# Performance work log

Measured on AMD Instinct MI355X. Metric: run time of the kernel, lower is better.

## Reference

```python
import jax, jax.numpy as jnp
import numpy as np

B, T_IN, T_OUT = 64, 512, 500
N_MEL, ENC_DIM, ATT_DIM = 80, 512, 128
ATT_RNN, DEC_RNN, PRENET = 1024, 1024, 256
N_FILT, KSIZE = 32, 31
PAD = (KSIZE - 1) // 2


def setup_inputs() -> dict:
    key = jax.random.key(0)
    ks = jax.random.split(key, 20)
    g = lambda i, shape, s: jax.random.normal(ks[i], shape, jnp.float32) * s
    return {
        'memory': g(0, (B, T_IN, ENC_DIM), 1.0),
        'decoder_inputs': g(1, (B, N_MEL, T_OUT), 1.0),
        'memory_lengths': jax.random.randint(ks[2], (B,), T_IN // 2, T_IN + 1).astype(jnp.int32),
        'prenet_w1': g(3, (PRENET, N_MEL), 0.05),
        'prenet_w2': g(4, (PRENET, PRENET), 0.05),
        'att_wih': g(5, (4 * ATT_RNN, PRENET + ENC_DIM), 0.02),
        'att_whh': g(6, (4 * ATT_RNN, ATT_RNN), 0.02),
        'att_bih': jnp.zeros((4 * ATT_RNN,), jnp.float32),
        'att_bhh': jnp.zeros((4 * ATT_RNN,), jnp.float32),
        'wq': g(7, (ATT_DIM, ATT_RNN), 0.03),
        'wm': g(8, (ATT_DIM, ENC_DIM), 0.03),
        'v': g(9, (ATT_DIM,), 0.05),
        'loc_conv': g(10, (N_FILT, 2, KSIZE), 0.05),
        'loc_dense': g(11, (ATT_DIM, N_FILT), 0.05),
        'dec_wih': g(12, (4 * DEC_RNN, ATT_RNN + ENC_DIM), 0.02),
        'dec_whh': g(13, (4 * DEC_RNN, DEC_RNN), 0.02),
        'dec_bih': jnp.zeros((4 * DEC_RNN,), jnp.float32),
        'dec_bhh': jnp.zeros((4 * DEC_RNN,), jnp.float32),
        'proj_w': g(14, (N_MEL, DEC_RNN + ENC_DIM), 0.02),
        'proj_b': jnp.zeros((N_MEL,), jnp.float32),
        'gate_w': g(15, (1, DEC_RNN + ENC_DIM), 0.02),
        'gate_b': jnp.zeros((1,), jnp.float32),
    }


def _lstm_cell(x, h, c, wih, whh, bih, bhh):
    gates = x @ wih.T + bih + h @ whh.T + bhh
    i, f, g, o = jnp.split(gates, 4, axis=-1)
    c_new = jax.nn.sigmoid(f) * c + jax.nn.sigmoid(i) * jnp.tanh(g)
    h_new = jax.nn.sigmoid(o) * jnp.tanh(c_new)
    return h_new, c_new


def _forward(memory, decoder_inputs, memory_lengths, prenet_w1, prenet_w2,
             att_wih, att_whh, att_bih, att_bhh, wq, wm, v, loc_conv, loc_dense,
             dec_wih, dec_whh, dec_bih, dec_bhh, proj_w, proj_b, gate_w, gate_b):
    # padding mask: True at padded encoder positions
    mask = jnp.arange(T_IN)[None, :] >= memory_lengths[:, None]  # [B, T_in]
    processed_memory = memory @ wm.T  # [B, T_in, ATT_DIM]

    # parse decoder inputs -> [T_out, B, N_MEL]; prepend all-zero go frame
    di = jnp.transpose(decoder_inputs, (2, 0, 1))
    di = jnp.concatenate([jnp.zeros((1, B, N_MEL), di.dtype), di], axis=0)

    # prenet (dropout p=0.5 is always active in the original; deterministic key)
    dk1, dk2 = jax.random.split(jax.random.key(42))
    x = jax.nn.relu(di @ prenet_w1.T)
    x = x * jax.random.bernoulli(dk1, 0.5, x.shape).astype(x.dtype) * 2.0
    x = jax.nn.relu(x @ prenet_w2.T)
    x = x * jax.random.bernoulli(dk2, 0.5, x.shape).astype(x.dtype) * 2.0  # [T_out+1, B, PRENET]

    def step(carry, x_t):
        ah, ac, dh, dc, aw, awc, ctx = carry
        # attention LSTM
        ah, ac = _lstm_cell(jnp.concatenate([x_t, ctx], -1), ah, ac,
                            att_wih, att_whh, att_bih, att_bhh)
        # location-sensitive attention
        awcat = jnp.stack([aw, awc], axis=1)  # [B, 2, T_in]
        loc = jax.lax.conv_general_dilated(awcat, loc_conv, (1,), [(PAD, PAD)],
                                           dimension_numbers=('NCH', 'OIH', 'NCH'))  # [B, F, T_in]
        loc = jnp.einsum('bft,af->bta', loc, loc_dense)  # [B, T_in, ATT_DIM]
        pq = (ah @ wq.T)[:, None, :]  # [B, 1, ATT_DIM]
        energies = jnp.tanh(pq + loc + processed_memory) @ v  # [B, T_in]
        energies = jnp.where(mask, -jnp.inf, energies)
        aw = jax.nn.softmax(energies, axis=1)
        ctx = jnp.einsum('bt,btd->bd', aw, memory)
        awc = awc + aw
        # decoder LSTM
        dh, dc = _lstm_cell(jnp.concatenate([ah, ctx], -1), dh, dc,
                            dec_wih, dec_whh, dec_bih, dec_bhh)
        dhc = jnp.concatenate([dh, ctx], -1)  # [B, DEC_RNN+ENC_DIM]
        mel = dhc @ proj_w.T + proj_b  # [B, N_MEL]
        gate = (dhc @ gate_w.T + gate_b)[:, 0]  # [B]
        return (ah, ac, dh, dc, aw, awc, ctx), (mel, gate, aw)

    z = lambda *s: jnp.zeros(s, jnp.float32)
    init = (z(B, ATT_RNN), z(B, ATT_RNN), z(B, DEC_RNN), z(B, DEC_RNN),
            z(B, T_IN), z(B, T_IN), z(B, ENC_DIM))
    _, (mels, gates, aws) = jax.lax.scan(step, init, x[:T_OUT])
    mel_outputs = jnp.transpose(mels, (1, 0, 2)).reshape(B, -1, N_MEL)  # [B, T_out, N_MEL]
    gate_outputs = gates.T  # [B, T_out]
    alignments = jnp.transpose(aws, (1, 0, 2))  # [B, T_out, T_in]
    return mel_outputs, gate_outputs, alignments


def reference(memory, decoder_inputs, memory_lengths, prenet_w1, prenet_w2,
              att_wih, att_whh, att_bih, att_bhh, wq, wm, v, loc_conv, loc_dense,
              dec_wih, dec_whh, dec_bih, dec_bhh, proj_w, proj_b, gate_w, gate_b):
    return _forward(memory, decoder_inputs, memory_lengths, prenet_w1, prenet_w2,
                    att_wih, att_whh, att_bih, att_bhh, wq, wm, v, loc_conv, loc_dense,
                    dec_wih, dec_whh, dec_bih, dec_bhh, proj_w, proj_b, gate_w, gate_b)
```

## Files before the change

kernel.cpp:

```cpp
#include <hip/hip_runtime.h>
#include <cstdint>
#include <cstddef>

#define NB    64
#define TIN   512
#define TOUT  500
#define NMEL  80
#define ENC   512
#define ATTD  128
#define ARNN  1024
#define DRNN  1024
#define PREN  256
#define NFILT 32
#define KSZ   31
#define CPAD  15

#define MEL_OFF  0
#define GATE_OFF 2560000
#define ALGN_OFF 2592000

#define X_SZ      8192000
#define PM_SZ     4194304
#define G1_SZ     1048576
#define G2_SZ     1048576
#define XATT_SZ   98304
#define XDEC_SZ   163840
#define AC_SZ     65536
#define DC_SZ     65536
#define AW_SZ     32768
#define AWC_SZ    32768
#define TAILH_SZ  49152
#define TAILL_SZ  49152
#define XDH_SZ    81920
#define XDL_SZ    81920
#define PQ_SZ     8192
#define EN_SZ     32768
#define MASK_N    8208384

#define K1TOT   1792
#define K2TOT   2560
#define NCH1    56
#define NCH2    80
#define PK1_N   14680064
#define PK2_N   20971520

typedef unsigned short u16;
typedef __attribute__((ext_vector_type(8))) short bf16x8;
typedef __attribute__((ext_vector_type(4))) float f32x4;

__device__ __forceinline__ uint32_t rotl32(uint32_t v, int r) { return (v << r) | (v >> (32 - r)); }

__device__ __forceinline__ float sigf(float x) { return 1.f / (1.f + __expf(-x)); }
__device__ __forceinline__ float tanhf_fast(float x) {
    float ax = fabsf(x);
    float t = 1.f - 2.f / (__expf(2.f * ax) + 1.f);
    return copysignf(t, x);
}

__device__ __forceinline__ void split1(float v, u16& h, u16& l) {
    uint32_t u = __float_as_uint(v);
    h = (u16)(u >> 16);
    float r = v - __uint_as_float(u & 0xFFFF0000u);
    uint32_t ru = __float_as_uint(r);
    ru += 0x7FFFu + ((ru >> 16) & 1u);
    l = (u16)(ru >> 16);
}

__device__ __forceinline__ void split8(float4 f0, float4 f1, bf16x8& h, bf16x8& l) {
    float v[8] = { f0.x, f0.y, f0.z, f0.w, f1.x, f1.y, f1.z, f1.w };
#pragma unroll
    for (int i = 0; i < 8; ++i) {
        uint32_t u = __float_as_uint(v[i]);
        h[i] = (short)(u >> 16);
        float r = v[i] - __uint_as_float(u & 0xFFFF0000u);
        uint32_t ru = __float_as_uint(r);
        ru += 0x7FFFu + ((ru >> 16) & 1u);
        l[i] = (short)(ru >> 16);
    }
}

#define MFMA16(a, b, c) __builtin_amdgcn_mfma_f32_16x16x32_bf16(a, b, c, 0, 0, 0)

__device__ void tf_block(uint32_t k1, uint32_t k2, uint32_t& x0, uint32_t& x1) {
    uint32_t ks0 = k1, ks1 = k2, ks2 = k1 ^ k2 ^ 0x1BD11BDAu;
    x0 += ks0; x1 += ks1;
#define TFR(r) { x0 += x1; x1 = rotl32(x1, r); x1 ^= x0; }
    TFR(13) TFR(15) TFR(26) TFR(6)   x0 += ks1; x1 += ks2 + 1u;
    TFR(17) TFR(29) TFR(16) TFR(24)  x0 += ks2; x1 += ks0 + 2u;
    TFR(13) TFR(15) TFR(26) TFR(6)   x0 += ks0; x1 += ks1 + 3u;
    TFR(17) TFR(29) TFR(16) TFR(24)  x0 += ks1; x1 += ks2 + 4u;
    TFR(13) TFR(15) TFR(26) TFR(6)   x0 += ks2; x1 += ks0 + 5u;
#undef TFR
}

__global__ __launch_bounds__(256) void mask_kernel(unsigned char* m1, unsigned char* m2) {
    int i = blockIdx.x * 256 + threadIdx.x;
    if (i >= MASK_N) return;
    uint32_t a0 = 0u, a1 = 0u; tf_block(0u, 42u, a0, a1);
    uint32_t b0 = 0u, b1 = 1u; tf_block(0u, 42u, b0, b1);
    uint32_t x0, x1;
    x0 = 0u; x1 = (uint32_t)i; tf_block(a0, a1, x0, x1);
    m1[i] = ((x0 ^ x1) >> 31) == 0u;
    x0 = 0u; x1 = (uint32_t)i; tf_block(b0, b1, x0, x1);
    m2[i] = ((x0 ^ x1) >> 31) == 0u;
}

__global__ __launch_bounds__(256) void prenet1_kernel(
    const float* __restrict__ dec_in, const float* __restrict__ w1,
    const unsigned char* __restrict__ m1, float* __restrict__ x)
{
    int r = blockIdx.x;
    int t = r >> 6, b = r & 63;
    int tid = threadIdx.x;
    __shared__ float ds[NMEL];
    if (tid < NMEL) ds[tid] = (t == 0) ? 0.f : dec_in[(size_t)b * 40000 + tid * 500 + (t - 1)];
    __syncthreads();
    float acc = 0.f;
    const float* w = w1 + tid * NMEL;
#pragma unroll
    for (int k = 0; k < NMEL; ++k) acc += ds[k] * w[k];
    acc = fmaxf(acc, 0.f);
    int flat = r * 256 + tid;
    x[flat] = m1[flat] ? acc * 2.f : 0.f;
}

__global__ __launch_bounds__(256) void prenet2_kernel(
    const float* __restrict__ w2, const unsigned char* __restrict__ m2, float* x)
{
    int r = blockIdx.x;
    int tid = threadIdx.x;
    __shared__ float xs[PREN];
    xs[tid] = x[r * 256 + tid];
    __syncthreads();
    float acc = 0.f;
    const float* w = w2 + tid * PREN;
#pragma unroll 8
    for (int k = 0; k < PREN; ++k) acc += xs[k] * w[k];
    acc = fmaxf(acc, 0.f);
    int flat = r * 256 + tid;
    x[flat] = m2[flat] ? acc * 2.f : 0.f;
}

__global__ __launch_bounds__(128) void pm_kernel(
    const float* __restrict__ memory, const float* __restrict__ wm, float* __restrict__ pm)
{
    int b = blockIdx.x, t = blockIdx.y;
    int tid = threadIdx.x;
    __shared__ float ms[ENC];
    for (int i = tid; i < ENC; i += 128) ms[i] = memory[(size_t)b * (TIN * ENC) + (size_t)t * ENC + i];
    __syncthreads();
    float acc = 0.f;
    const float* w = wm + tid * ENC;
#pragma unroll 8
    for (int k = 0; k < ENC; ++k) acc += ms[k] * w[k];
    pm[(size_t)b * (TIN * ATTD) + t * ATTD + tid] = acc;
}

__global__ __launch_bounds__(256) void wpack_kernel(
    const float* __restrict__ w1, int K1, const float* __restrict__ w2, int K2,
    u16* __restrict__ dst)
{
    const int K = K1 + K2;
    int idx = blockIdx.x * 256 + threadIdx.x;
    if (idx >= 4096 * K) return;
    int n = idx / K, k = idx % K;
    float v = (k < K1) ? w1[n * K1 + k] : w2[n * K2 + (k - K1)];
    u16 h, l;
    split1(v, h, l);
    int tile = n >> 4, kc = k >> 5;
    int lane = (n & 15) + (((k & 31) >> 3) << 4);
    size_t off = ((size_t)(tile * (K >> 5) + kc) * 2) * 512 + lane * 8 + (k & 7);
    dst[off] = h;
    dst[off + 512] = l;
}

struct SmemGemm { float Xs[32][68]; float Ws[32][68]; };

__device__ void gemm_phase(
    const float* __restrict__ X1, int ldx1, int kx1,
    const float* __restrict__ X2, int ldx2,
    const float* __restrict__ W1, int ldw1, int kw1,
    const float* __restrict__ W2, int ldw2,
    float* __restrict__ outp, int Kq, int blk, SmemGemm& s)
{
    const int tid = threadIdx.x;
    const int n0 = (blk & 63) * 64;
    const int ks = blk >> 6;
    const int kbeg = ks * Kq;
    const int tn = tid & 15, tm = tid >> 4;
    float acc[4][4];
#pragma unroll
    for (int i = 0; i < 4; ++i)
#pragma unroll
        for (int j = 0; j < 4; ++j) acc[i][j] = 0.f;

#pragma unroll 1
    for (int k0 = kbeg; k0 < kbeg + Kq; k0 += 32) {
#pragma unroll
        for (int i = 0; i < 8; ++i) {
            int flat = i * 256 + tid;
            int m = flat >> 5, c = flat & 31;
            int k = k0 + c;
            s.Xs[c][m] = (k < kx1) ? X1[m * ldx1 + k] : X2[m * ldx2 + (k - kx1)];
        }
#pragma unroll
        for (int i = 0; i < 8; ++i) {
            int flat = i * 256 + tid;
            int r = flat >> 5, c = flat & 31;
            int k = k0 + c;
            int n = n0 + r;
            s.Ws[c][r] = (k < kw1) ? W1[n * ldw1 + k] : W2[n * ldw2 + (k - kw1)];
        }
        __syncthreads();
#pragma unroll
        for (int kk = 0; kk < 32; ++kk) {
            float4 xv = *(const float4*)&s.Xs[kk][tm * 4];
            float4 wv = *(const float4*)&s.Ws[kk][tn * 4];
            float xr[4] = { xv.x, xv.y, xv.z, xv.w };
            float wr[4] = { wv.x, wv.y, wv.z, wv.w };
#pragma unroll
            for (int i = 0; i < 4; ++i)
#pragma unroll
                for (int j = 0; j < 4; ++j) acc[i][j] += xr[i] * wr[j];
        }
        __syncthreads();
    }
    float* o = outp + (size_t)ks * 64 * 4096;
#pragma unroll
    for (int i = 0; i < 4; ++i)
#pragma unroll
        for (int j = 0; j < 4; ++j)
            o[(tm * 4 + i) * 4096 + (n0 + tn * 4 + j)] = acc[i][j];
}

__global__ __launch_bounds__(256, 2) void pair_gemm(
    const float* __restrict__ xcat_dec,
    const float* __restrict__ dec_wih, const float* __restrict__ dec_whh,
    float* __restrict__ g2,
    const float* __restrict__ x, const float* __restrict__ xcat_att,
    const float* __restrict__ att_wih, const float* __restrict__ att_whh,
    float* __restrict__ g1, int t)
{
    __shared__ __align__(16) SmemGemm sm;
    const int blk = blockIdx.x;
    if (blk < 256) {
        if (t < 0) return;
        gemm_phase(xcat_dec, 2560, 2560, xcat_dec, 2560,
                   dec_wih, 1536, 1536, dec_whh, 1024, g2, 640, blk, sm);
    } else {
        const int tn = t + 1;
        if (tn >= TOUT) return;
        gemm_phase(x + (size_t)tn * (NB * PREN), PREN, PREN, xcat_att, 1536,
                   att_wih, 768, 768, att_whh, 1024, g1, 448, blk - 256, sm);
    }
}

__device__ __forceinline__ void mfma_tile_run(
    const u16* __restrict__ Ah, const u16* __restrict__ Al, int aoff,
    const float* __restrict__ xr,
    const u16* __restrict__ bp, int kc_beg, int nchunk, int kc_wrap_at, int kc_wrap_to,
    f32x4& acc, int lane)
{
    const int kg = lane >> 4;
#pragma unroll 4
    for (int i = 0; i < nchunk; ++i) {
        int kc = kc_beg + i;
        if (kc >= kc_wrap_at) kc = kc_wrap_to + (kc - kc_wrap_at);
        const int k = kc * 32 + kg * 8;
        bf16x8 ah, al;
        if (xr && k < 256) {
            float4 f0 = *(const float4*)(xr + k);
            float4 f1 = *(const float4*)(xr + k + 4);
            split8(f0, f1, ah, al);
        } else {
            ah = *(const bf16x8*)(Ah + (k - aoff));
            al = *(const bf16x8*)(Al + (k - aoff));
        }
        const u16* c0 = bp + (size_t)kc * 1024;
        bf16x8 bh = *(const bf16x8*)c0;
        bf16x8 bl = *(const bf16x8*)(c0 + 512);
        acc = MFMA16(ah, bh, acc); acc = MFMA16(ah, bl, acc); acc = MFMA16(al, bh, acc);
    }
}

__device__ __forceinline__ void mfma_store(float* o, f32x4 acc, int tile, int wave, int lane)
{
    const int n0 = tile * 16;
    const int mbase = wave * 16 + (lane >> 4) * 4;
    const int lr = lane & 15;
#pragma unroll
    for (int r = 0; r < 4; ++r)
        o[(mbase + r) * 4096 + n0 + lr] = acc[r];
}

__device__ void energies_body(
    int b, int tc,
    const float* __restrict__ aw, const float* __restrict__ awc,
    const float* __restrict__ lc, const float* __restrict__ ld,
    const float* __restrict__ vvec, const float* __restrict__ pq,
    const float* __restrict__ pm, float* __restrict__ energ)
{
    const int t0 = tc * 64;
    const int tid = threadIdx.x;
    __shared__ float awin[96], awcin[96];
    __shared__ float lcs[NFILT * 62];
    __shared__ float locs[64 * 33];
    __shared__ float pqs[ATTD], vs[ATTD];
    __shared__ float ldm[ATTD * 33];

    for (int i = tid; i < 94; i += 256) {
        int t = t0 + i - CPAD;
        bool ok = (t >= 0 && t < TIN);
        awin[i]  = ok ? aw[b * TIN + t]  : 0.f;
        awcin[i] = ok ? awc[b * TIN + t] : 0.f;
    }
    for (int i = tid; i < NFILT * 62; i += 256) lcs[i] = lc[i];
    for (int i = tid; i < ATTD * NFILT; i += 256) ldm[(i >> 5) * 33 + (i & 31)] = ld[i];
    if (tid < ATTD) { pqs[tid] = pq[b * ATTD + tid]; vs[tid] = vvec[tid]; }
    __syncthreads();

    for (int idx = tid; idx < 64 * 32; idx += 256) {
        int tl = idx >> 5, f = idx & 31;
        const float* w0 = lcs + f * 62;
        float s = 0.f;
#pragma unroll
        for (int k = 0; k < KSZ; ++k)
            s += awin[tl + k] * w0[k] + awcin[tl + k] * w0[31 + k];
        locs[tl * 33 + f] = s;
    }
    __syncthreads();

    const int tl = tid >> 2, q = tid & 3;
    const int a0 = q * 32;
    const float* pmrow = pm + (size_t)b * (TIN * ATTD) + (size_t)(t0 + tl) * ATTD + a0;
    const float* lt = locs + tl * 33;
    float4 pv[8];
#pragma unroll
    for (int u = 0; u < 8; ++u) pv[u] = *(const float4*)&pmrow[u * 4];
    float e = 0.f;
#pragma unroll
    for (int aa = 0; aa < 32; ++aa) {
        int a = a0 + aa;
        float sv = pqs[a] + ((const float*)pv)[aa];
        const float* lrow = ldm + a * 33;
#pragma unroll
        for (int f = 0; f < NFILT; ++f) sv += lt[f] * lrow[f];
        e += vs[a] * tanhf_fast(sv);
    }
    e += __shfl_xor(e, 1);
    e += __shfl_xor(e, 2);
    if (q == 0) energ[b * TIN + t0 + tl] = e;
}

__global__ __launch_bounds__(256) void fused_mid(
    const float* __restrict__ aw, const float* __restrict__ awc,
    const float* __restrict__ lc, const float* __restrict__ ld,
    const float* __restrict__ vvec, const float* __restrict__ pq,
    const float* __restrict__ pm, float* __restrict__ energ,
    const u16* __restrict__ xdech, const u16* __restrict__ xdecl,
    const u16* __restrict__ pk2, float* __restrict__ g2, int t)
{
    const int blk = blockIdx.x;
    if (t < 0) return;
    if (blk < 512) {
        energies_body(blk >> 3, blk & 7, aw, awc, lc, ld, vvec, pq, pm, energ);
        return;
    }
    const int tid = threadIdx.x;
    const int wave = tid >> 6, lane = tid & 63;
    const int mrow = wave * 16 + (lane & 15);
    f32x4 acc = {0.f, 0.f, 0.f, 0.f};
    const int r = blk - 512;
    const int tile = r & 255, ks = r >> 8;
    const u16* bp = pk2 + (size_t)tile * NCH2 * 1024 + lane * 8;
    mfma_tile_run(xdech + mrow * 2560, xdecl + mrow * 2560, 0, nullptr,
                  bp, ks == 0 ? 0 : 48, 32, 1000, 0, acc, lane);
    mfma_store(g2 + (size_t)ks * 262144, acc, tile, wave, lane);
}

__global__ __launch_bounds__(256) void fused_sm(
    const float* __restrict__ energ, const int* __restrict__ mlen,
    const float* __restrict__ memory,
    float* __restrict__ aw, float* __restrict__ awc,
    float* __restrict__ out_align, int t,
    float* __restrict__ xcat_att, float* __restrict__ xcat_dec,
    u16* __restrict__ tailh, u16* __restrict__ taill,
    u16* __restrict__ xdech, u16* __restrict__ xdecl,
    const float* __restrict__ x,
    const u16* __restrict__ pk1, float* __restrict__ g1)
{
    const int blk = blockIdx.x;
    const int tid = threadIdx.x;

    if (blk >= 512) {
        const int tn = t + 1;
        if (tn >= TOUT) return;
        const int wave = tid >> 6, lane = tid & 63;
        const int mrow = wave * 16 + (lane & 15);
        f32x4 acc = {0.f, 0.f, 0.f, 0.f};
        const int r = blk - 512;
        const int tile = r & 255, ks = r >> 8;
        const u16* bp = pk1 + (size_t)tile * NCH1 * 1024 + lane * 8;
        const float* xr = x + ((size_t)tn * 64 + mrow) * 256;
        mfma_tile_run(tailh + mrow * 1536, taill + mrow * 1536, 256, xr,
                      bp, ks == 0 ? 24 : 44, 20, 56, 0, acc, lane);
        mfma_store(g1 + (size_t)ks * 262144, acc, tile, wave, lane);
        return;
    }

    if (t < 0) return;
    const int b = blk >> 3, dq = blk & 7;
    const int len = mlen[b];
    __shared__ float es[TIN];
    __shared__ float red[256];

    float e1 = (tid < len) ? energ[b * TIN + tid] : -INFINITY;
    float e2 = (tid + 256 < len) ? energ[b * TIN + tid + 256] : -INFINITY;
    red[tid] = fmaxf(e1, e2);
    __syncthreads();
    for (int s = 128; s > 0; s >>= 1) {
        if (tid < s) red[tid] = fmaxf(red[tid], red[tid + s]);
        __syncthreads();
    }
    const float mx = red[0];
    __syncthreads();
    float p1 = __expf(e1 - mx);
    float p2 = __expf(e2 - mx);
    red[tid] = p1 + p2;
    __syncthreads();
    for (int s = 128; s > 0; s >>= 1) {
        if (tid < s) red[tid] += red[tid + s];
        __syncthreads();
    }
    const float inv = 1.f / red[0];
    p1 *= inv; p2 *= inv;
    es[tid] = p1; es[tid + 256] = p2;
    __syncthreads();

    if (tid < 64) {
        int tt = dq * 64 + tid;
        float p = es[tt];
        aw[b * TIN + tt] = p;
        awc[b * TIN + tt] += p;
        out_align[(size_t)b * (TOUT * TIN) + (size_t)t * TIN + tt] = p;
    }

    const int d = dq * 64 + (tid & 63), th = tid >> 6;
    const float* mb = memory + (size_t)b * (TIN * ENC);
    float accv = 0.f;
#pragma unroll 4
    for (int tt = th * 128; tt < th * 128 + 128; ++tt)
        accv += es[tt] * mb[(size_t)tt * ENC + d];
    red[tid] = accv;
    __syncthreads();
    if (tid < 64) {
        float cv = (red[tid] + red[tid + 64]) + (red[tid + 128] + red[tid + 192]);
        int dd = dq * 64 + tid;
        xcat_att[b * 1536 + dd] = cv;
        xcat_dec[b * 2560 + 1024 + dd] = cv;
        u16 h, l; split1(cv, h, l);
        tailh[b * 1536 + dd] = h;        taill[b * 1536 + dd] = l;
        xdech[b * 2560 + 1024 + dd] = h; xdecl[b * 2560 + 1024 + dd] = l;
    }
}

__global__ __launch_bounds__(256) void gemm_late(
    const u16* __restrict__ xdech, const u16* __restrict__ xdecl,
    const u16* __restrict__ pk2, float* __restrict__ g2,
    const u16* __restrict__ tailh, const u16* __restrict__ taill,
    const u16* __restrict__ pk1, float* __restrict__ g1, int t)
{
    const int blk = blockIdx.x;
    const int tid = threadIdx.x;
    const int wave = tid >> 6, lane = tid & 63;
    const int mrow = wave * 16 + (lane & 15);
    f32x4 acc = {0.f, 0.f, 0.f, 0.f};

    if (blk < 256) {
        if (t < 0) return;
        const int tile = blk;
        const u16* bp = pk2 + (size_t)tile * NCH2 * 1024 + lane * 8;
        mfma_tile_run(xdech + mrow * 2560, xdecl + mrow * 2560, 0, nullptr,
                      bp, 32, 16, 1000, 0, acc, lane);
        mfma_store(g2 + (size_t)2 * 262144, acc, tile, wave, lane);
    } else {
        const int tn = t + 1;
        if (tn >= TOUT) return;
        const int tile = blk - 256;
        const u16* bp = pk1 + (size_t)tile * NCH1 * 1024 + lane * 8;
        mfma_tile_run(tailh + mrow * 1536, taill + mrow * 1536, 256, nullptr,
                      bp, 8, 16, 1000, 0, acc, lane);
        mfma_store(g1 + (size_t)2 * 262144, acc, tile, wave, lane);
    }
}

__global__ __launch_bounds__(256) void pair_pw(
    const float* __restrict__ g1, const float* __restrict__ att_bih, const float* __restrict__ att_bhh,
    float* __restrict__ ac, float* __restrict__ xcat_att, float* __restrict__ xcat_dec,
    const float* __restrict__ wq, float* __restrict__ pq,
    const float* __restrict__ g2, const float* __restrict__ dec_bih, const float* __restrict__ dec_bhh,
    float* __restrict__ dc, const float* __restrict__ proj_w, const float* __restrict__ proj_b,
    const float* __restrict__ gate_w, const float* __restrict__ gate_b,
    float* __restrict__ out,
    u16* __restrict__ tailh, u16* __restrict__ taill,
    u16* __restrict__ xdech, u16* __restrict__ xdecl,
    int nsplit, int t)
{
    const int tid = threadIdx.x;
    __shared__ float sbuf[1536];
    __shared__ float red[256];

    if (blockIdx.x < 64) {
        if (t >= TOUT) return;
        const int b = blockIdx.x;
#pragma unroll
        for (int q = 0; q < 4; ++q) {
            int j = q * 256 + tid;
            float gi = att_bih[j] + att_bhh[j];
            float gf = att_bih[1024 + j] + att_bhh[1024 + j];
            float gg = att_bih[2048 + j] + att_bhh[2048 + j];
            float go = att_bih[3072 + j] + att_bhh[3072 + j];
            for (int s = 0; s < nsplit; ++s) {
                const float* g = g1 + (size_t)s * 262144 + b * 4096;
                gi += g[j]; gf += g[1024 + j]; gg += g[2048 + j]; go += g[3072 + j];
            }
            float c = sigf(gf) * ac[b * 1024 + j] + sigf(gi) * tanhf_fast(gg);
            float h = sigf(go) * tanhf_fast(c);
            ac[b * 1024 + j] = c;
            xcat_att[b * 1536 + 512 + j] = h;
            xcat_dec[b * 2560 + j] = h;
            u16 hh, hl; split1(h, hh, hl);
            tailh[b * 1536 + 512 + j] = hh;  taill[b * 1536 + 512 + j] = hl;
            xdech[b * 2560 + j] = hh;        xdecl[b * 2560 + j] = hl;
            sbuf[j] = h;
        }
        __syncthreads();
        const int a = tid & 127, half = tid >> 7;
        const float* wr = wq + a * 1024 + half * 512;
        const float* hh = sbuf + half * 512;
        float s0 = 0.f, s1 = 0.f, s2 = 0.f, s3 = 0.f;
#pragma unroll 4
        for (int k = 0; k < 512; k += 16) {
            float4 w0 = *(const float4*)&wr[k],      h0 = *(const float4*)&hh[k];
            float4 w1 = *(const float4*)&wr[k + 4],  h1 = *(const float4*)&hh[k + 4];
            float4 w2 = *(const float4*)&wr[k + 8],  h2 = *(const float4*)&hh[k + 8];
            float4 w3 = *(const float4*)&wr[k + 12], h3 = *(const float4*)&hh[k + 12];
            s0 += h0.x * w0.x + h0.y * w0.y + h0.z * w0.z + h0.w * w0.w;
            s1 += h1.x * w1.x + h1.y * w1.y + h1.z * w1.z + h1.w * w1.w;
            s2 += h2.x * w2.x + h2.y * w2.y + h2.z * w2.z + h2.w * w2.w;
            s3 += h3.x * w3.x + h3.y * w3.y + h3.z * w3.z + h3.w * w3.w;
        }
        red[tid] = (s0 + s1) + (s2 + s3);
        __syncthreads();
        if (half == 0) pq[b * 128 + a] = red[a] + red[a + 128];
    } else {
        if (t < 1) return;
        const int b = blockIdx.x - 64;
        const int ts = t - 1;
#pragma unroll
        for (int q = 0; q < 4; ++q) {
            int j = q * 256 + tid;
            float gi = dec_bih[j] + dec_bhh[j];
            float gf = dec_bih[1024 + j] + dec_bhh[1024 + j];
            float gg = dec_bih[2048 + j] + dec_bhh[2048 + j];
            float go = dec_bih[3072 + j] + dec_bhh[3072 + j];
            for (int s = 0; s < nsplit; ++s) {
                const float* g = g2 + (size_t)s * 262144 + b * 4096;
                gi += g[j]; gf += g[1024 + j]; gg += g[2048 + j]; go += g[3072 + j];
            }
            float c = sigf(gf) * dc[b * 1024 + j] + sigf(gi) * tanhf_fast(gg);
            float h = sigf(go) * tanhf_fast(c);
            dc[b * 1024 + j] = c;
            xcat_dec[b * 2560 + 1536 + j] = h;
            u16 hh, hl; split1(h, hh, hl);
            xdech[b * 2560 + 1536 + j] = hh;  xdecl[b * 2560 + 1536 + j] = hl;
            sbuf[j] = h;
        }
        for (int i = tid; i < 512; i += 256) sbuf[1024 + i] = xcat_dec[b * 2560 + 1024 + i];
        __syncthreads();
        const int o = tid >> 1, half = tid & 1;
        float accv = 0.f;
        if (o <= 80) {
            const float* w = (o < 80) ? (proj_w + o * 1536) : gate_w;
            const float* sv = sbuf + half * 768;
            const float* wv = w + half * 768;
            float s0 = 0.f, s1 = 0.f, s2 = 0.f, s3 = 0.f;
#pragma unroll 4
            for (int k = 0; k < 768; k += 16) {
                float4 a0 = *(const float4*)&sv[k],      b0 = *(const float4*)&wv[k];
                float4 a1 = *(const float4*)&sv[k + 4],  b1 = *(const float4*)&wv[k + 4];
                float4 a2 = *(const float4*)&sv[k + 8],  b2 = *(const float4*)&wv[k + 8];
                float4 a3 = *(const float4*)&sv[k + 12], b3 = *(const float4*)&wv[k + 12];
                s0 += a0.x * b0.x + a0.y * b0.y + a0.z * b0.z + a0.w * b0.w;
                s1 += a1.x * b1.x + a1.y * b1.y + a1.z * b1.z + a1.w * b1.w;
                s2 += a2.x * b2.x + a2.y * b2.y + a2.z * b2.z + a2.w * b2.w;
                s3 += a3.x * b3.x + a3.y * b3.y + a3.z * b3.z + a3.w * b3.w;
            }
            accv = (s0 + s1) + (s2 + s3);
        }
        red[tid] = accv;
        __syncthreads();
        if (half == 0 && o <= 80) {
            float r = red[tid] + red[tid + 1];
            if (o < 80)
                out[MEL_OFF + (size_t)b * (TOUT * NMEL) + (size_t)ts * NMEL + o] = r + proj_b[o];
            else
                out[GATE_OFF + (size_t)b * TOUT + ts] = r + gate_b[0];
        }
    }
}

__global__ __launch_bounds__(256) void energies_kernel(
    const float* __restrict__ aw, const float* __restrict__ awc,
    const float* __restrict__ lc, const float* __restrict__ ld,
    const float* __restrict__ vvec, const float* __restrict__ pq,
    const float* __restrict__ pm, float* __restrict__ energ)
{
    energies_body(blockIdx.x >> 3, blockIdx.x & 7, aw, awc, lc, ld, vvec, pq, pm, energ);
}

__global__ __launch_bounds__(256) void softmax_ctx_kernel(
    const float* __restrict__ energ, const int* __restrict__ mlen,
    const float* __restrict__ memory,
    float* __restrict__ aw, float* __restrict__ awc,
    float* __restrict__ out_align, int t_step,
    float* __restrict__ xcat_att, float* __restrict__ xcat_dec,
    u16* __restrict__ tailh, u16* __restrict__ taill,
    u16* __restrict__ xdech, u16* __restrict__ xdecl)
{
    const int b = blockIdx.x >> 3, dq = blockIdx.x & 7;
    const int tid = threadIdx.x;
    const int len = mlen[b];
    __shared__ float es[TIN];
    __shared__ float red[256];

    float e1 = (tid < len) ? energ[b * TIN + tid] : -INFINITY;
    float e2 = (tid + 256 < len) ? energ[b * TIN + tid + 256] : -INFINITY;
    red[tid] = fmaxf(e1, e2);
    __syncthreads();
    for (int s = 128; s > 0; s >>= 1) {
        if (tid < s) red[tid] = fmaxf(red[tid], red[tid + s]);
        __syncthreads();
    }
    const float mx = red[0];
    __syncthreads();
    float p1 = __expf(e1 - mx);
    float p2 = __expf(e2 - mx);
    red[tid] = p1 + p2;
    __syncthreads();
    for (int s = 128; s > 0; s >>= 1) {
        if (tid < s) red[tid] += red[tid + s];
        __syncthreads();
    }
    const float inv = 1.f / red[0];
    p1 *= inv; p2 *= inv;
    es[tid] = p1; es[tid + 256] = p2;
    __syncthreads();

    if (tid < 64) {
        int tt = dq * 64 + tid;
        float p = es[tt];
        aw[b * TIN + tt] = p;
        awc[b * TIN + tt] += p;
        out_align[(size_t)b * (TOUT * TIN) + (size_t)t_step * TIN + tt] = p;
    }

    const int d = dq * 64 + (tid & 63), th = tid >> 6;
    const float* mb = memory + (size_t)b * (TIN * ENC);
    float accv = 0.f;
#pragma unroll 4
    for (int tt = th * 128; tt < th * 128 + 128; ++tt)
        accv += es[tt] * mb[(size_t)tt * ENC + d];
    red[tid] = accv;
    __syncthreads();
    if (tid < 64) {
        float cv = (red[tid] + red[tid + 64]) + (red[tid + 128] + red[tid + 192]);
        int dd = dq * 64 + tid;
        xcat_att[b * 1536 + dd] = cv;
        xcat_dec[b * 2560 + 1024 + dd] = cv;
        u16 h, l; split1(cv, h, l);
        tailh[b * 1536 + dd] = h;        taill[b * 1536 + dd] = l;
        xdech[b * 2560 + 1024 + dd] = h; xdecl[b * 2560 + 1024 + dd] = l;
    }
}

extern "C" void kernel_launch(void* const* d_in, const int* in_sizes, int n_in,
                              void* d_out, int out_size, void* d_ws, size_t ws_size,
                              hipStream_t stream) {
    const float* memory   = (const float*)d_in[0];
    const float* dec_in   = (const float*)d_in[1];
    const int*   mlen     = (const int*)d_in[2];
    const float* pw1      = (const float*)d_in[3];
    const float* pw2      = (const float*)d_in[4];
    const float* att_wih  = (const float*)d_in[5];
    const float* att_whh  = (const float*)d_in[6];
    const float* att_bih  = (const float*)d_in[7];
    const float* att_bhh  = (const float*)d_in[8];
    const float* wq       = (const float*)d_in[9];
    const float* wm       = (const float*)d_in[10];
    const float* v        = (const float*)d_in[11];
    const float* loc_conv = (const float*)d_in[12];
    const float* loc_dense= (const float*)d_in[13];
    const float* dec_wih  = (const float*)d_in[14];
    const float* dec_whh  = (const float*)d_in[15];
    const float* dec_bih  = (const float*)d_in[16];
    const float* dec_bhh  = (const float*)d_in[17];
    const float* proj_w   = (const float*)d_in[18];
    const float* proj_b   = (const float*)d_in[19];
    const float* gate_w   = (const float*)d_in[20];
    const float* gate_b   = (const float*)d_in[21];
    float* out = (float*)d_out;

    float* x        = (float*)d_ws;
    float* pm       = x + X_SZ;
    float* g1       = pm + PM_SZ;
    float* g2       = g1 + G1_SZ;
    float* xcat_att = g2 + G2_SZ;
    float* xcat_dec = xcat_att + XATT_SZ;
    float* ac       = xcat_dec + XDEC_SZ;
    float* dc       = ac + AC_SZ;
    float* aw       = dc + DC_SZ;
    float* awc      = aw + AW_SZ;
    float* tailh_f  = awc + AWC_SZ;
    float* taill_f  = tailh_f + TAILH_SZ;
    float* xdech_f  = taill_f + TAILL_SZ;
    float* xdecl_f  = xdech_f + XDH_SZ;
    float* pq       = xdecl_f + XDL_SZ;
    float* energ    = pq + PQ_SZ;
    unsigned char* m1 = (unsigned char*)(energ + EN_SZ);
    unsigned char* m2 = m1 + MASK_N;
    u16* pk1 = (u16*)(m2 + MASK_N);
    u16* pk2 = pk1 + PK1_N;

    u16* tailh = (u16*)tailh_f;  u16* taill = (u16*)taill_f;
    u16* xdech = (u16*)xdech_f;  u16* xdecl = (u16*)xdecl_f;

    size_t need_base = (size_t)(m2 + MASK_N - (unsigned char*)d_ws);
    size_t need_full = (size_t)((unsigned char*)(pk2 + PK2_N) - (unsigned char*)d_ws);
    if (ws_size < need_base) return;
    const bool use_mfma = (ws_size >= need_full);
    const int nsplit = use_mfma ? 3 : 4;

    size_t state_floats = (size_t)XATT_SZ + XDEC_SZ + AC_SZ + DC_SZ + AW_SZ + AWC_SZ
                        + TAILH_SZ + TAILL_SZ + XDH_SZ + XDL_SZ;
    hipMemsetAsync(xcat_att, 0, state_floats * sizeof(float), stream);

    mask_kernel<<<(MASK_N + 255) / 256, 256, 0, stream>>>(m1, m2);
    prenet1_kernel<<<TOUT * NB, 256, 0, stream>>>(dec_in, pw1, m1, x);
    prenet2_kernel<<<TOUT * NB, 256, 0, stream>>>(pw2, m2, x);
    pm_kernel<<<dim3(NB, TIN), 128, 0, stream>>>(memory, wm, pm);
    if (use_mfma) {
        wpack_kernel<<<(4096 * K1TOT + 255) / 256, 256, 0, stream>>>(att_wih, 768, att_whh, 1024, pk1);
        wpack_kernel<<<(4096 * K2TOT + 255) / 256, 256, 0, stream>>>(dec_wih, 1536, dec_whh, 1024, pk2);
    }

    float* out_align = out + ALGN_OFF;

    if (use_mfma) {
        fused_sm<<<1024, 256, 0, stream>>>(energ, mlen, memory, aw, awc, out_align, -1,
                                           xcat_att, xcat_dec, tailh, taill, xdech, xdecl,
                                           x, pk1, g1);
        gemm_late<<<512, 256, 0, stream>>>(xdech, xdecl, pk2, g2, tailh, taill, pk1, g1, -1);
    } else {
        pair_gemm<<<512, 256, 0, stream>>>(xcat_dec, dec_wih, dec_whh, g2,
                                           x, xcat_att, att_wih, att_whh, g1, -1);
    }

    for (int t = 0; t < TOUT; ++t) {
        pair_pw<<<128, 256, 0, stream>>>(g1, att_bih, att_bhh, ac, xcat_att, xcat_dec, wq, pq,
                                         g2, dec_bih, dec_bhh, dc, proj_w, proj_b,
                                         gate_w, gate_b, out, tailh, taill, xdech, xdecl,
                                         nsplit, t);
        if (use_mfma) {
            fused_mid<<<1024, 256, 0, stream>>>(aw, awc, loc_conv, loc_dense, v, pq, pm, energ,
                                                xdech, xdecl, pk2, g2, t);
            fused_sm<<<1024, 256, 0, stream>>>(energ, mlen, memory, aw, awc, out_align, t,
                                               xcat_att, xcat_dec, tailh, taill, xdech, xdecl,
                                               x, pk1, g1);
            gemm_late<<<512, 256, 0, stream>>>(xdech, xdecl, pk2, g2, tailh, taill, pk1, g1, t);
        } else {
            energies_kernel<<<512, 256, 0, stream>>>(aw, awc, loc_conv, loc_dense, v, pq, pm, energ);
            softmax_ctx_kernel<<<512, 256, 0, stream>>>(energ, mlen, memory, aw, awc, out_align, t,
                                                        xcat_att, xcat_dec, tailh, taill, xdech, xdecl);
            pair_gemm<<<512, 256, 0, stream>>>(xcat_dec, dec_wih, dec_whh, g2,
                                               x, xcat_att, att_wih, att_whh, g1, t);
        }
    }
    pair_pw<<<128, 256, 0, stream>>>(g1, att_bih, att_bhh, ac, xcat_att, xcat_dec, wq, pq,
                                     g2, dec_bih, dec_bhh, dc, proj_w, proj_b,
                                     gate_w, gate_b, out, tailh, taill, xdech, xdecl,
                                     nsplit, TOUT);
}
```

Measured before the change: 50.24 ms.

## Move mel/gate projection into fused_mid and double softmax-context block split

The per-batch mel/gate projection moves out of the decoder-LSTM pointwise blocks of pair_pw into 64 extra blocks of fused_mid, so it runs alongside the energies and decoder GEMM work instead of serialising the critical pointwise kernel. fused_sm also splits the context reduction across 16 column slices per batch instead of 8, launching 1536 blocks, to spread the memory-bound context reads over more CUs. Block index ranges are reordered so the GEMM blocks come first in both kernels. A trailing fused_mid launch writes the final projection, and the softmax is now recomputed redundantly in twice as many blocks.

```diff
diff --git a/kernel.cpp b/kernel.cpp
--- a/kernel.cpp
+++ b/kernel.cpp
@@ -352,30 +352,81 @@
     if (q == 0) energ[b * TIN + t0 + tl] = e;
 }
 
+__device__ void proj_body(
+    int b, int ts, const float* __restrict__ xcat_dec,
+    const float* __restrict__ proj_w, const float* __restrict__ proj_b,
+    const float* __restrict__ gate_w, const float* __restrict__ gate_b,
+    float* __restrict__ out)
+{
+    __shared__ float s[1536];
+    __shared__ float red2[256];
+    const int tid = threadIdx.x;
+    const float* xd = xcat_dec + b * 2560;
+    for (int i = tid; i < 1024; i += 256) s[i] = xd[1536 + i];
+    for (int i = tid; i < 512; i += 256)  s[1024 + i] = xd[1024 + i];
+    __syncthreads();
+    const int o = tid >> 1, half = tid & 1;
+    float accv = 0.f;
+    if (o <= 80) {
+        const float* w = (o < 80) ? (proj_w + o * 1536) : gate_w;
+        const float* sv = s + half * 768;
+        const float* wv = w + half * 768;
+        float s0 = 0.f, s1 = 0.f, s2 = 0.f, s3 = 0.f;
+#pragma unroll 4
+        for (int k = 0; k < 768; k += 16) {
+            float4 a0 = *(const float4*)&sv[k],      b0 = *(const float4*)&wv[k];
+            float4 a1 = *(const float4*)&sv[k + 4],  b1 = *(const float4*)&wv[k + 4];
+            float4 a2 = *(const float4*)&sv[k + 8],  b2 = *(const float4*)&wv[k + 8];
+            float4 a3 = *(const float4*)&sv[k + 12], b3 = *(const float4*)&wv[k + 12];
+            s0 += a0.x * b0.x + a0.y * b0.y + a0.z * b0.z + a0.w * b0.w;
+            s1 += a1.x * b1.x + a1.y * b1.y + a1.z * b1.z + a1.w * b1.w;
+            s2 += a2.x * b2.x + a2.y * b2.y + a2.z * b2.z + a2.w * b2.w;
+            s3 += a3.x * b3.x + a3.y * b3.y + a3.z * b3.z + a3.w * b3.w;
+        }
+        accv = (s0 + s1) + (s2 + s3);
+    }
+    red2[tid] = accv;
+    __syncthreads();
+    if (half == 0 && o <= 80) {
+        float r = red2[tid] + red2[tid + 1];
+        if (o < 80)
+            out[MEL_OFF + (size_t)b * (TOUT * NMEL) + (size_t)ts * NMEL + o] = r + proj_b[o];
+        else
+            out[GATE_OFF + (size_t)b * TOUT + ts] = r + gate_b[0];
+    }
+}
+
 __global__ __launch_bounds__(256) void fused_mid(
     const float* __restrict__ aw, const float* __restrict__ awc,
     const float* __restrict__ lc, const float* __restrict__ ld,
     const float* __restrict__ vvec, const float* __restrict__ pq,
     const float* __restrict__ pm, float* __restrict__ energ,
     const u16* __restrict__ xdech, const u16* __restrict__ xdecl,
-    const u16* __restrict__ pk2, float* __restrict__ g2, int t)
+    const u16* __restrict__ pk2, float* __restrict__ g2,
+    const float* __restrict__ xcat_dec,
+    const float* __restrict__ proj_w, const float* __restrict__ proj_b,
+    const float* __restrict__ gate_w, const float* __restrict__ gate_b,
+    float* __restrict__ out, int t)
 {
     const int blk = blockIdx.x;
-    if (t < 0) return;
+    const int tid = threadIdx.x;
     if (blk < 512) {
-        energies_body(blk >> 3, blk & 7, aw, awc, lc, ld, vvec, pq, pm, energ);
-        return;
-    }
-    const int tid = threadIdx.x;
-    const int wave = tid >> 6, lane = tid & 63;
-    const int mrow = wave * 16 + (lane & 15);
-    f32x4 acc = {0.f, 0.f, 0.f, 0.f};
-    const int r = blk - 512;
-    const int tile = r & 255, ks = r >> 8;
-    const u16* bp = pk2 + (size_t)tile * NCH2 * 1024 + lane * 8;
-    mfma_tile_run(xdech + mrow * 2560, xdecl + mrow * 2560, 0, nullptr,
-                  bp, ks == 0 ? 0 : 48, 32, 1000, 0, acc, lane);
-    mfma_store(g2 + (size_t)ks * 262144, acc, tile, wave, lane);
+        if (t < 0 || t >= TOUT) return;
+        const int wave = tid >> 6, lane = tid & 63;
+        const int mrow = wave * 16 + (lane & 15);
+        f32x4 acc = {0.f, 0.f, 0.f, 0.f};
+        const int tile = blk & 255, ks = blk >> 8;
+        const u16* bp = pk2 + (size_t)tile * NCH2 * 1024 + lane * 8;
+        mfma_tile_run(xdech + mrow * 2560, xdecl + mrow * 2560, 0, nullptr,
+                      bp, ks == 0 ? 0 : 48, 32, 1000, 0, acc, lane);
+        mfma_store(g2 + (size_t)ks * 262144, acc, tile, wave, lane);
+    } else if (blk < 1024) {
+        if (t < 0 || t >= TOUT) return;
+        energies_body((blk - 512) >> 3, (blk - 512) & 7, aw, awc, lc, ld, vvec, pq, pm, energ);
+    } else {
+        if (t < 1) return;
+        proj_body(blk - 1024, t - 1, xcat_dec, proj_w, proj_b, gate_w, gate_b, out);
+    }
 }
 
 __global__ __launch_bounds__(256) void fused_sm(
@@ -392,14 +443,13 @@
     const int blk = blockIdx.x;
     const int tid = threadIdx.x;
 
-    if (blk >= 512) {
+    if (blk < 512) {
         const int tn = t + 1;
         if (tn >= TOUT) return;
         const int wave = tid >> 6, lane = tid & 63;
         const int mrow = wave * 16 + (lane & 15);
         f32x4 acc = {0.f, 0.f, 0.f, 0.f};
-        const int r = blk - 512;
-        const int tile = r & 255, ks = r >> 8;
+        const int tile = blk & 255, ks = blk >> 8;
         const u16* bp = pk1 + (size_t)tile * NCH1 * 1024 + lane * 8;
         const float* xr = x + ((size_t)tn * 64 + mrow) * 256;
         mfma_tile_run(tailh + mrow * 1536, taill + mrow * 1536, 256, xr,
@@ -408,8 +458,9 @@
         return;
     }
 
-    if (t < 0) return;
-    const int b = blk >> 3, dq = blk & 7;
+    if (t < 0 || t >= TOUT) return;
+    const int q = blk - 512;
+    const int b = q >> 4, dq = q & 15;
     const int len = mlen[b];
     __shared__ float es[TIN];
     __shared__ float red[256];
@@ -437,25 +488,26 @@
     es[tid] = p1; es[tid + 256] = p2;
     __syncthreads();
 
-    if (tid < 64) {
-        int tt = dq * 64 + tid;
+    if (tid < 32) {
+        int tt = dq * 32 + tid;
         float p = es[tt];
         aw[b * TIN + tt] = p;
         awc[b * TIN + tt] += p;
         out_align[(size_t)b * (TOUT * TIN) + (size_t)t * TIN + tt] = p;
     }
 
-    const int d = dq * 64 + (tid & 63), th = tid >> 6;
+    const int d = dq * 32 + (tid & 31), th = tid >> 5;
     const float* mb = memory + (size_t)b * (TIN * ENC);
     float accv = 0.f;
-#pragma unroll 4
-    for (int tt = th * 128; tt < th * 128 + 128; ++tt)
+#pragma unroll 8
+    for (int tt = th * 64; tt < th * 64 + 64; ++tt)
         accv += es[tt] * mb[(size_t)tt * ENC + d];
     red[tid] = accv;
     __syncthreads();
-    if (tid < 64) {
-        float cv = (red[tid] + red[tid + 64]) + (red[tid + 128] + red[tid + 192]);
-        int dd = dq * 64 + tid;
+    if (tid < 32) {
+        float cv = ((red[tid] + red[tid + 32]) + (red[tid + 64] + red[tid + 96]))
+                 + ((red[tid + 128] + red[tid + 160]) + (red[tid + 192] + red[tid + 224]));
+        int dd = dq * 32 + tid;
         xcat_att[b * 1536 + dd] = cv;
         xcat_dec[b * 2560 + 1024 + dd] = cv;
         u16 h, l; split1(cv, h, l);
@@ -499,9 +551,7 @@
     float* __restrict__ ac, float* __restrict__ xcat_att, float* __restrict__ xcat_dec,
     const float* __restrict__ wq, float* __restrict__ pq,
     const float* __restrict__ g2, const float* __restrict__ dec_bih, const float* __restrict__ dec_bhh,
-    float* __restrict__ dc, const float* __restrict__ proj_w, const float* __restrict__ proj_b,
-    const float* __restrict__ gate_w, const float* __restrict__ gate_b,
-    float* __restrict__ out,
+    float* __restrict__ dc,
     u16* __restrict__ tailh, u16* __restrict__ taill,
     u16* __restrict__ xdech, u16* __restrict__ xdecl,
     int nsplit, int t)
@@ -556,7 +606,6 @@
     } else {
         if (t < 1) return;
         const int b = blockIdx.x - 64;
-        const int ts = t - 1;
 #pragma unroll
         for (int q = 0; q < 4; ++q) {
             int j = q * 256 + tid;
@@ -574,38 +623,6 @@
             xcat_dec[b * 2560 + 1536 + j] = h;
             u16 hh, hl; split1(h, hh, hl);
             xdech[b * 2560 + 1536 + j] = hh;  xdecl[b * 2560 + 1536 + j] = hl;
-            sbuf[j] = h;
-        }
-        for (int i = tid; i < 512; i += 256) sbuf[1024 + i] = xcat_dec[b * 2560 + 1024 + i];
-        __syncthreads();
-        const int o = tid >> 1, half = tid & 1;
-        float accv = 0.f;
-        if (o <= 80) {
-            const float* w = (o < 80) ? (proj_w + o * 1536) : gate_w;
-            const float* sv = sbuf + half * 768;
-            const float* wv = w + half * 768;
-            float s0 = 0.f, s1 = 0.f, s2 = 0.f, s3 = 0.f;
-#pragma unroll 4
-            for (int k = 0; k < 768; k += 16) {
-                float4 a0 = *(const float4*)&sv[k],      b0 = *(const float4*)&wv[k];
-                float4 a1 = *(const float4*)&sv[k + 4],  b1 = *(const float4*)&wv[k + 4];
-                float4 a2 = *(const float4*)&sv[k + 8],  b2 = *(const float4*)&wv[k + 8];
-                float4 a3 = *(const float4*)&sv[k + 12], b3 = *(const float4*)&wv[k + 12];
-                s0 += a0.x * b0.x + a0.y * b0.y + a0.z * b0.z + a0.w * b0.w;
-                s1 += a1.x * b1.x + a1.y * b1.y + a1.z * b1.z + a1.w * b1.w;
-                s2 += a2.x * b2.x + a2.y * b2.y + a2.z * b2.z + a2.w * b2.w;
-                s3 += a3.x * b3.x + a3.y * b3.y + a3.z * b3.z + a3.w * b3.w;
-            }
-            accv = (s0 + s1) + (s2 + s3);
-        }
-        red[tid] = accv;
-        __syncthreads();
-        if (half == 0 && o <= 80) {
-            float r = red[tid] + red[tid + 1];
-            if (o < 80)
-                out[MEL_OFF + (size_t)b * (TOUT * NMEL) + (size_t)ts * NMEL + o] = r + proj_b[o];
-            else
-                out[GATE_OFF + (size_t)b * TOUT + ts] = r + gate_b[0];
         }
     }
 }
@@ -617,6 +634,16 @@
     const float* __restrict__ pm, float* __restrict__ energ)
 {
     energies_body(blockIdx.x >> 3, blockIdx.x & 7, aw, awc, lc, ld, vvec, pq, pm, energ);
+}
+
+__global__ __launch_bounds__(256) void proj_kernel_fb(
+    const float* __restrict__ xcat_dec,
+    const float* __restrict__ proj_w, const float* __restrict__ proj_b,
+    const float* __restrict__ gate_w, const float* __restrict__ gate_b,
+    float* __restrict__ out, int t)
+{
+    if (t < 1) return;
+    proj_body(blockIdx.x, t - 1, xcat_dec, proj_w, proj_b, gate_w, gate_b, out);
 }
 
 __global__ __launch_bounds__(256) void softmax_ctx_kernel(
@@ -757,7 +784,7 @@
     float* out_align = out + ALGN_OFF;
 
     if (use_mfma) {
-        fused_sm<<<1024, 256, 0, stream>>>(energ, mlen, memory, aw, awc, out_align, -1,
+        fused_sm<<<1536, 256, 0, stream>>>(energ, mlen, memory, aw, awc, out_align, -1,
                                            xcat_att, xcat_dec, tailh, taill, xdech, xdecl,
                                            x, pk1, g1);
         gemm_late<<<512, 256, 0, stream>>>(xdech, xdecl, pk2, g2, tailh, taill, pk1, g1, -1);
@@ -768,17 +795,18 @@
 
     for (int t = 0; t < TOUT; ++t) {
         pair_pw<<<128, 256, 0, stream>>>(g1, att_bih, att_bhh, ac, xcat_att, xcat_dec, wq, pq,
-                                         g2, dec_bih, dec_bhh, dc, proj_w, proj_b,
-                                         gate_w, gate_b, out, tailh, taill, xdech, xdecl,
-                                         nsplit, t);
+                                         g2, dec_bih, dec_bhh, dc,
+                                         tailh, taill, xdech, xdecl, nsplit, t);
         if (use_mfma) {
-            fused_mid<<<1024, 256, 0, stream>>>(aw, awc, loc_conv, loc_dense, v, pq, pm, energ,
-                                                xdech, xdecl, pk2, g2, t);
-            fused_sm<<<1024, 256, 0, stream>>>(energ, mlen, memory, aw, awc, out_align, t,
+            fused_mid<<<1088, 256, 0, stream>>>(aw, awc, loc_conv, loc_dense, v, pq, pm, energ,
+                                                xdech, xdecl, pk2, g2,
+                                                xcat_dec, proj_w, proj_b, gate_w, gate_b, out, t);
+            fused_sm<<<1536, 256, 0, stream>>>(energ, mlen, memory, aw, awc, out_align, t,
                                                xcat_att, xcat_dec, tailh, taill, xdech, xdecl,
                                                x, pk1, g1);
             gemm_late<<<512, 256, 0, stream>>>(xdech, xdecl, pk2, g2, tailh, taill, pk1, g1, t);
         } else {
+            proj_kernel_fb<<<64, 256, 0, stream>>>(xcat_dec, proj_w, proj_b, gate_w, gate_b, out, t);
             energies_kernel<<<512, 256, 0, stream>>>(aw, awc, loc_conv, loc_dense, v, pq, pm, energ);
             softmax_ctx_kernel<<<512, 256, 0, stream>>>(energ, mlen, memory, aw, awc, out_align, t,
                                                         xcat_att, xcat_dec, tailh, taill, xdech, xdecl);
@@ -787,7 +815,12 @@
         }
     }
     pair_pw<<<128, 256, 0, stream>>>(g1, att_bih, att_bhh, ac, xcat_att, xcat_dec, wq, pq,
-                                     g2, dec_bih, dec_bhh, dc, proj_w, proj_b,
-                                     gate_w, gate_b, out, tailh, taill, xdech, xdecl,
-                                     nsplit, TOUT);
-}
+                                     g2, dec_bih, dec_bhh, dc,
+                                     tailh, taill, xdech, xdecl, nsplit, TOUT);
+    if (use_mfma)
+        fused_mid<<<1088, 256, 0, stream>>>(aw, awc, loc_conv, loc_dense, v, pq, pm, energ,
+                                            xdech, xdecl, pk2, g2,
+                                            xcat_dec, proj_w, proj_b, gate_w, gate_b, out, TOUT);
+    else
+        proj_kernel_fb<<<64, 256, 0, stream>>>(xcat_dec, proj_w, proj_b, gate_w, gate_b, out, TOUT);
+}
```

Result: slower. 61.42 ms (+22.2%).
